# Optimization experiments

Measured on AMD Instinct MI355X. Metric: run time of the kernel, lower is better.

## Reference

```python
import jax, jax.numpy as jnp
import numpy as np

B, T, EMBED_DIM, HEAD_SIZE = 512, 256, 384, 64


def setup_inputs() -> dict:
    key = jax.random.key(0)
    k1, k2, k3, k4 = jax.random.split(key, 4)
    x = jax.random.normal(k1, (B, T, EMBED_DIM), dtype=jnp.float32)
    # torch nn.Linear(embed_dim, head_size, bias=False): y = x @ W.T with W [out,in].
    # We store W as [in, out] so the projection is x @ W.
    Wq = jax.random.normal(k2, (EMBED_DIM, HEAD_SIZE), dtype=jnp.float32) * 0.02
    Wk = jax.random.normal(k3, (EMBED_DIM, HEAD_SIZE), dtype=jnp.float32) * 0.02
    Wv = jax.random.normal(k4, (EMBED_DIM, HEAD_SIZE), dtype=jnp.float32) * 0.02
    return {"x": x, "Wq": Wq, "Wk": Wk, "Wv": Wv}


def reference(x, Wq, Wk, Wv):
    # x: [B, T, E]
    Tlen = x.shape[1]
    E = x.shape[2]
    q = x @ Wq  # [B, T, H]
    k = x @ Wk  # [B, T, H]
    v = x @ Wv  # [B, T, H]
    wei = jnp.einsum("bqh,bkh->bqk", q, k)  # [B, T, T] raw scores (no pre-softmax scale!)
    causal = jnp.tril(jnp.ones((Tlen, Tlen), dtype=bool))
    wei = jnp.where(causal, wei, jnp.float32(-jnp.inf))
    wei = jax.nn.softmax(wei, axis=-1)
    # NOTE: original module divides by sqrt(embed_dim) AFTER softmax (faithful quirk).
    wei = wei / jnp.sqrt(jnp.asarray(E, wei.dtype))
    # dropout is identity in eval/deterministic mode
    out = jnp.einsum("bqk,bkh->bqh", wei, v)  # [B, T, H]
    return out
```

## Files before the change

kernel.cpp:

```cpp
#include <hip/hip_runtime.h>


typedef _Float16 half8 __attribute__((ext_vector_type(8)));
typedef float f32x4 __attribute__((ext_vector_type(4)));

#define MFMA16(a, b, c) __builtin_amdgcn_mfma_f32_16x16x32_f16(a, b, c, 0, 0, 0)

#define QOFF 0
#define QSTR 72
#define KOFF 18432
#define VOFF 36864
#define VSTR 264
#define POFF 53760
#define PSTR 24
#define LDS_F16 59904
#define LDS_BYTES (LDS_F16 * 2)

__global__ void pack_w_kernel(const float* __restrict__ Wq, const float* __restrict__ Wk,
                              const float* __restrict__ Wv, _Float16* __restrict__ wp) {
    int tid = blockIdx.x * 256 + threadIdx.x;
    if (tid >= 12 * 12 * 64 * 8) return;
    int i    = tid & 7;
    int l    = (tid >> 3) & 63;
    int ctks = tid >> 9;
    int ct   = ctks % 12;
    int ks   = ctks / 12;
    int k    = ks * 32 + 8 * (l >> 4) + i;
    int c    = l & 15;
    const float* src;
    int h;
    if (ct < 4)      { src = Wq; h = ct * 16 + c; }
    else if (ct < 8) { src = Wk; h = (ct - 4) * 16 + c; }
    else             { src = Wv; h = (ct - 8) * 16 + c; }
    wp[tid] = (_Float16)src[k * 64 + h];
}

__global__ __launch_bounds__(512) void fused_kernel(
        const float* __restrict__ x, const _Float16* __restrict__ wp,
        float* __restrict__ out) {
    extern __shared__ _Float16 lds[];
    const int b = blockIdx.x;
    const int w = threadIdx.x >> 6, l = threadIdx.x & 63;
    const int c = l & 15, g = l >> 4;

    {
        const float* base0 = x + (b * 256 + w * 32 + c) * 384;
        const float* base1 = base0 + 16 * 384;
        f32x4 acc[2][12] = {};
        float4 buf[2][4];
        buf[0][0] = *(const float4*)(base0 + 8 * g);
        buf[0][1] = *(const float4*)(base0 + 8 * g + 4);
        buf[0][2] = *(const float4*)(base1 + 8 * g);
        buf[0][3] = *(const float4*)(base1 + 8 * g + 4);
#pragma unroll
        for (int s = 0; s < 12; ++s) {
            const int cb = s & 1, nb = cb ^ 1;
            if (s < 11) {
                int o = (s + 1) * 32 + 8 * g;
                buf[nb][0] = *(const float4*)(base0 + o);
                buf[nb][1] = *(const float4*)(base0 + o + 4);
                buf[nb][2] = *(const float4*)(base1 + o);
                buf[nb][3] = *(const float4*)(base1 + o + 4);
            }
            half8 a0, a1;
#pragma unroll
            for (int e = 0; e < 4; ++e) {
                a0[e]     = (_Float16)buf[cb][0][e];
                a0[e + 4] = (_Float16)buf[cb][1][e];
                a1[e]     = (_Float16)buf[cb][2][e];
                a1[e + 4] = (_Float16)buf[cb][3][e];
            }
#pragma unroll
            for (int ct = 0; ct < 12; ++ct) {
                half8 bf = *(const half8*)(wp + ((s * 12 + ct) * 64 + l) * 8);
                acc[0][ct] = MFMA16(a0, bf, acc[0][ct]);
                acc[1][ct] = MFMA16(a1, bf, acc[1][ct]);
            }
        }
#pragma unroll
        for (int rt = 0; rt < 2; ++rt) {
            int r0 = w * 32 + rt * 16;
#pragma unroll
            for (int ct = 0; ct < 12; ++ct) {
                if (ct < 4) {
                    int h = ct * 16 + c;
#pragma unroll
                    for (int r = 0; r < 4; ++r)
                        lds[QOFF + (r0 + 4 * g + r) * QSTR + h] = (_Float16)acc[rt][ct][r];
                } else if (ct < 8) {
                    int h = (ct - 4) * 16 + c;
#pragma unroll
                    for (int r = 0; r < 4; ++r)
                        lds[KOFF + (r0 + 4 * g + r) * QSTR + h] = (_Float16)acc[rt][ct][r];
                } else {
                    int h  = (ct - 8) * 16 + c;
                    int t0 = r0 + 4 * g;
                    union { ushort4 u; _Float16 hh[4]; } pk;
#pragma unroll
                    for (int r = 0; r < 4; ++r) pk.hh[r] = (_Float16)acc[rt][ct][r];
                    *(ushort4*)&lds[VOFF + h * VSTR + t0] = pk.u;
                }
            }
        }
    }
    __syncthreads();

    const float qk_scale = 0.05103103630798288f;
    float* ob = out + b * 16384;
    _Float16* pw = &lds[POFF + w * 768];

#pragma unroll
    for (int j = 0; j < 2; ++j) {
        const int qt = j ? (15 - w) : w;
        const int r0 = qt * 16;
        half8 aq0 = *(const half8*)&lds[QOFF + (r0 + c) * QSTR + 8 * g];
        half8 aq1 = *(const half8*)&lds[QOFF + (r0 + c) * QSTR + 32 + 8 * g];

        f32x4 oac[4] = {};
        float lsum[4] = {0.f, 0.f, 0.f, 0.f};
        const int nkk = (qt >> 1) + 1;

        for (int kk = 0; kk < nkk; ++kk) {
            const int c0 = kk * 32;
            f32x4 S[2];
#pragma unroll
            for (int t = 0; t < 2; ++t) {
                const _Float16* kp = &lds[KOFF + (c0 + 16 * t + c) * QSTR + 8 * g];
                half8 bk0 = *(const half8*)kp;
                half8 bk1 = *(const half8*)(kp + 32);
                f32x4 z = {};
                z = MFMA16(aq0, bk0, z);
                z = MFMA16(aq1, bk1, z);
                S[t] = z;
            }
            float p[2][4];
            if (kk == nkk - 1) {
#pragma unroll
                for (int t = 0; t < 2; ++t)
#pragma unroll
                    for (int r = 0; r < 4; ++r) {
                        float sv = (c0 + 16 * t + c > r0 + 4 * g + r) ? -1e30f
                                                                      : S[t][r] - 6.0f;
                        p[t][r] = __expf(sv);
                        lsum[r] += p[t][r];
                    }
            } else {
#pragma unroll
                for (int t = 0; t < 2; ++t)
#pragma unroll
                    for (int r = 0; r < 4; ++r) {
                        p[t][r] = __expf(S[t][r] - 6.0f);
                        lsum[r] += p[t][r];
                    }
            }
#pragma unroll
            for (int t = 0; t < 2; ++t)
#pragma unroll
                for (int r = 0; r < 4; ++r)
                    pw[t * 384 + (4 * g + r) * PSTR + c] = (_Float16)p[t][r];
            asm volatile("s_waitcnt lgkmcnt(0)" ::: "memory");
            half8 pa = *(const half8*)&pw[(g >> 1) * 384 + c * PSTR + 8 * (g & 1)];
#pragma unroll
            for (int ht = 0; ht < 4; ++ht) {
                half8 bv = *(const half8*)&lds[VOFF + (16 * ht + c) * VSTR + c0 + 8 * g];
                oac[ht] = MFMA16(pa, bv, oac[ht]);
            }
        }
#pragma unroll
        for (int r = 0; r < 4; ++r) {
            float ls = lsum[r];
            ls += __shfl_xor(ls, 1);
            ls += __shfl_xor(ls, 2);
            ls += __shfl_xor(ls, 4);
            ls += __shfl_xor(ls, 8);
            float inv = qk_scale / ls;
#pragma unroll
            for (int ht = 0; ht < 4; ++ht)
                ob[(r0 + 4 * g + r) * 64 + 16 * ht + c] = oac[ht][r] * inv;
        }
    }
}

extern "C" void kernel_launch(void* const* d_in, const int* in_sizes, int n_in,
                              void* d_out, int out_size, void* d_ws, size_t ws_size,
                              hipStream_t stream) {
    const float* x  = (const float*)d_in[0];
    const float* Wq = (const float*)d_in[1];
    const float* Wk = (const float*)d_in[2];
    const float* Wv = (const float*)d_in[3];
    float* out = (float*)d_out;
    _Float16* wp = (_Float16*)d_ws;

    (void)hipFuncSetAttribute((const void*)fused_kernel,
                              hipFuncAttributeMaxDynamicSharedMemorySize, LDS_BYTES);

    pack_w_kernel<<<288, 256, 0, stream>>>(Wq, Wk, Wv, wp);
    fused_kernel<<<512, 512, LDS_BYTES, stream>>>(x, wp, out);
}
```

Measured before the change: 333.3 us.

## Stage weights in LDS, swizzle Q/K/V layouts, transpose S to keep P in registers

Projection weights are now staged into LDS in two halves instead of being read from global memory per MFMA. x loads move to a three-deep buffer. Q/K/V go into XOR-swizzled, unpadded LDS layouts, which lowers bank conflicts and LDS footprint, and launch bounds ask for two blocks per CU. The attention part computes transposed scores (K·Q) so P can be repacked with cross-lane shuffles instead of a round trip through LDS. It also skips the fully masked half-tile on the diagonal and writes the output with vectorized stores. In exchange it adds extra barriers during the projection, shuffle overhead, and register pressure from the occupancy hint.

```diff
diff --git a/kernel.cpp b/kernel.cpp
--- a/kernel.cpp
+++ b/kernel.cpp
@@ -2,19 +2,32 @@
 
 
 typedef _Float16 half8 __attribute__((ext_vector_type(8)));
+typedef __fp16 fp16x2 __attribute__((ext_vector_type(2)));
 typedef float f32x4 __attribute__((ext_vector_type(4)));
 
 #define MFMA16(a, b, c) __builtin_amdgcn_mfma_f32_16x16x32_f16(a, b, c, 0, 0, 0)
 
 #define QOFF 0
-#define QSTR 72
-#define KOFF 18432
-#define VOFF 36864
-#define VSTR 264
-#define POFF 53760
-#define PSTR 24
-#define LDS_F16 59904
+#define KOFF 16384
+#define VOFF 32768
+#define LDS_F16 49152
 #define LDS_BYTES (LDS_F16 * 2)
+
+__device__ __forceinline__ int qk_idx(int row, int h) {
+    return row * 64 + (h & 7) + ((((h >> 3) ^ row) & 7) << 3);
+}
+__device__ __forceinline__ int vt_idx(int h, int key) {
+    return h * 256 + (key & 7) + ((((key >> 3) ^ (h & 7)) & 31) << 3);
+}
+
+__device__ __forceinline__ unsigned long long pkquad(float a, float b, float c, float d) {
+    fp16x2 lo = __builtin_amdgcn_cvt_pkrtz(a, b);
+    fp16x2 hi = __builtin_amdgcn_cvt_pkrtz(c, d);
+    unsigned ulo, uhi;
+    __builtin_memcpy(&ulo, &lo, 4);
+    __builtin_memcpy(&uhi, &hi, 4);
+    return ((unsigned long long)uhi << 32) | ulo;
+}
 
 __global__ void pack_w_kernel(const float* __restrict__ Wq, const float* __restrict__ Wk,
                               const float* __restrict__ Wv, _Float16* __restrict__ wp) {
@@ -24,8 +37,8 @@
     int l    = (tid >> 3) & 63;
     int ctks = tid >> 9;
     int ct   = ctks % 12;
-    int ks   = ctks / 12;
-    int k    = ks * 32 + 8 * (l >> 4) + i;
+    int s    = ctks / 12;
+    int k    = s * 32 + 8 * (l >> 4) + i;
     int c    = l & 15;
     const float* src;
     int h;
@@ -35,71 +48,84 @@
     wp[tid] = (_Float16)src[k * 64 + h];
 }
 
-__global__ __launch_bounds__(512) void fused_kernel(
+__global__ __launch_bounds__(512, 2) void fused_kernel(
         const float* __restrict__ x, const _Float16* __restrict__ wp,
         float* __restrict__ out) {
     extern __shared__ _Float16 lds[];
     const int b = blockIdx.x;
-    const int w = threadIdx.x >> 6, l = threadIdx.x & 63;
+    const int tid = threadIdx.x;
+    const int w = tid >> 6, l = tid & 63;
     const int c = l & 15, g = l >> 4;
 
-    {
-        const float* base0 = x + (b * 256 + w * 32 + c) * 384;
-        const float* base1 = base0 + 16 * 384;
-        f32x4 acc[2][12] = {};
-        float4 buf[2][4];
-        buf[0][0] = *(const float4*)(base0 + 8 * g);
-        buf[0][1] = *(const float4*)(base0 + 8 * g + 4);
-        buf[0][2] = *(const float4*)(base1 + 8 * g);
-        buf[0][3] = *(const float4*)(base1 + 8 * g + 4);
-#pragma unroll
-        for (int s = 0; s < 12; ++s) {
-            const int cb = s & 1, nb = cb ^ 1;
-            if (s < 11) {
-                int o = (s + 1) * 32 + 8 * g;
-                buf[nb][0] = *(const float4*)(base0 + o);
-                buf[nb][1] = *(const float4*)(base0 + o + 4);
-                buf[nb][2] = *(const float4*)(base1 + o);
-                buf[nb][3] = *(const float4*)(base1 + o + 4);
-            }
-            half8 a0, a1;
-#pragma unroll
-            for (int e = 0; e < 4; ++e) {
-                a0[e]     = (_Float16)buf[cb][0][e];
-                a0[e + 4] = (_Float16)buf[cb][1][e];
-                a1[e]     = (_Float16)buf[cb][2][e];
-                a1[e + 4] = (_Float16)buf[cb][3][e];
-            }
-#pragma unroll
-            for (int ct = 0; ct < 12; ++ct) {
-                half8 bf = *(const half8*)(wp + ((s * 12 + ct) * 64 + l) * 8);
-                acc[0][ct] = MFMA16(a0, bf, acc[0][ct]);
-                acc[1][ct] = MFMA16(a1, bf, acc[1][ct]);
-            }
-        }
-#pragma unroll
-        for (int rt = 0; rt < 2; ++rt) {
-            int r0 = w * 32 + rt * 16;
-#pragma unroll
-            for (int ct = 0; ct < 12; ++ct) {
-                if (ct < 4) {
-                    int h = ct * 16 + c;
-#pragma unroll
-                    for (int r = 0; r < 4; ++r)
-                        lds[QOFF + (r0 + 4 * g + r) * QSTR + h] = (_Float16)acc[rt][ct][r];
-                } else if (ct < 8) {
-                    int h = (ct - 4) * 16 + c;
-#pragma unroll
-                    for (int r = 0; r < 4; ++r)
-                        lds[KOFF + (r0 + 4 * g + r) * QSTR + h] = (_Float16)acc[rt][ct][r];
-                } else {
-                    int h  = (ct - 8) * 16 + c;
-                    int t0 = r0 + 4 * g;
-                    union { ushort4 u; _Float16 hh[4]; } pk;
-#pragma unroll
-                    for (int r = 0; r < 4; ++r) pk.hh[r] = (_Float16)acc[rt][ct][r];
-                    *(ushort4*)&lds[VOFF + h * VSTR + t0] = pk.u;
+    const float* base0 = x + (b * 256 + w * 32 + c) * 384;
+    const float* base1 = base0 + 16 * 384;
+    f32x4 acc[2][12] = {};
+
+#pragma unroll
+    for (int i = 0; i < 9; ++i) {
+        int ch = i * 512 + tid;
+        *(uint4*)&lds[ch * 8] = *(const uint4*)(wp + ch * 8);
+    }
+    __syncthreads();
+
+    f32x4 xb[3][4];
+#define XLOAD(bi, s) do { const float* p0_ = base0 + (s) * 32 + 8 * g; \
+        const float* p1_ = base1 + (s) * 32 + 8 * g; \
+        xb[bi][0] = *(const f32x4*)p0_; xb[bi][1] = *(const f32x4*)(p0_ + 4); \
+        xb[bi][2] = *(const f32x4*)p1_; xb[bi][3] = *(const f32x4*)(p1_ + 4); } while (0)
+
+    XLOAD(0, 0);
+    XLOAD(1, 1);
+#pragma unroll
+    for (int s = 0; s < 12; ++s) {
+        if (s == 6) {
+            __syncthreads();
+#pragma unroll
+            for (int i = 0; i < 9; ++i) {
+                int ch = i * 512 + tid;
+                *(uint4*)&lds[ch * 8] = *(const uint4*)(wp + 36864 + ch * 8);
+            }
+            __syncthreads();
+        }
+        const int cb = s % 3;
+        if (s < 10) XLOAD((s + 2) % 3, s + 2);
+        half8 a0, a1;
+#pragma unroll
+        for (int e = 0; e < 4; ++e) {
+            a0[e]     = (_Float16)xb[cb][0][e];
+            a0[e + 4] = (_Float16)xb[cb][1][e];
+            a1[e]     = (_Float16)xb[cb][2][e];
+            a1[e + 4] = (_Float16)xb[cb][3][e];
+        }
+#pragma unroll
+        for (int ct = 0; ct < 12; ++ct) {
+            half8 bf = *(const half8*)&lds[((s % 6) * 12 + ct) * 512 + l * 8];
+            acc[0][ct] = MFMA16(a0, bf, acc[0][ct]);
+            acc[1][ct] = MFMA16(a1, bf, acc[1][ct]);
+        }
+    }
+    __syncthreads();
+
+#pragma unroll
+    for (int rt = 0; rt < 2; ++rt) {
+        int r0 = w * 32 + rt * 16;
+#pragma unroll
+        for (int ct = 0; ct < 12; ++ct) {
+            if (ct < 8) {
+                int off = (ct < 4) ? QOFF : KOFF;
+                int h = (ct & 3) * 16 + c;
+#pragma unroll
+                for (int r = 0; r < 4; ++r) {
+                    int row = r0 + 4 * g + r;
+                    lds[off + qk_idx(row, h)] = (_Float16)acc[rt][ct][r];
                 }
+            } else {
+                int h  = (ct - 8) * 16 + c;
+                int t0 = r0 + 4 * g;
+                union { ushort4 u; _Float16 hh[4]; } pk;
+#pragma unroll
+                for (int r = 0; r < 4; ++r) pk.hh[r] = (_Float16)acc[rt][ct][r];
+                *(ushort4*)&lds[VOFF + vt_idx(h, t0)] = pk.u;
             }
         }
     }
@@ -107,76 +133,81 @@
 
     const float qk_scale = 0.05103103630798288f;
     float* ob = out + b * 16384;
-    _Float16* pw = &lds[POFF + w * 768];
 
 #pragma unroll
     for (int j = 0; j < 2; ++j) {
         const int qt = j ? (15 - w) : w;
         const int r0 = qt * 16;
-        half8 aq0 = *(const half8*)&lds[QOFF + (r0 + c) * QSTR + 8 * g];
-        half8 aq1 = *(const half8*)&lds[QOFF + (r0 + c) * QSTR + 32 + 8 * g];
-
-        f32x4 oac[4] = {};
-        float lsum[4] = {0.f, 0.f, 0.f, 0.f};
+        const int qrow = r0 + c;
+        half8 aq0 = *(const half8*)&lds[QOFF + qrow * 64 + (((g ^ qrow) & 7) << 3)];
+        half8 aq1 = *(const half8*)&lds[QOFF + qrow * 64 + ((((g + 4) ^ qrow) & 7) << 3)];
+
+        f32x4 oacT[4] = {};
+        float lsum = 0.f;
         const int nkk = (qt >> 1) + 1;
 
         for (int kk = 0; kk < nkk; ++kk) {
             const int c0 = kk * 32;
-            f32x4 S[2];
-#pragma unroll
-            for (int t = 0; t < 2; ++t) {
-                const _Float16* kp = &lds[KOFF + (c0 + 16 * t + c) * QSTR + 8 * g];
-                half8 bk0 = *(const half8*)kp;
-                half8 bk1 = *(const half8*)(kp + 32);
-                f32x4 z = {};
-                z = MFMA16(aq0, bk0, z);
-                z = MFMA16(aq1, bk1, z);
-                S[t] = z;
-            }
-            float p[2][4];
-            if (kk == nkk - 1) {
-#pragma unroll
-                for (int t = 0; t < 2; ++t)
-#pragma unroll
-                    for (int r = 0; r < 4; ++r) {
-                        float sv = (c0 + 16 * t + c > r0 + 4 * g + r) ? -1e30f
-                                                                      : S[t][r] - 6.0f;
-                        p[t][r] = __expf(sv);
-                        lsum[r] += p[t][r];
-                    }
-            } else {
-#pragma unroll
-                for (int t = 0; t < 2; ++t)
-#pragma unroll
-                    for (int r = 0; r < 4; ++r) {
-                        p[t][r] = __expf(S[t][r] - 6.0f);
-                        lsum[r] += p[t][r];
-                    }
-            }
-#pragma unroll
-            for (int t = 0; t < 2; ++t)
-#pragma unroll
-                for (int r = 0; r < 4; ++r)
-                    pw[t * 384 + (4 * g + r) * PSTR + c] = (_Float16)p[t][r];
-            asm volatile("s_waitcnt lgkmcnt(0)" ::: "memory");
-            half8 pa = *(const half8*)&pw[(g >> 1) * 384 + c * PSTR + 8 * (g & 1)];
+            const bool diag  = (kk == nkk - 1);
+            const bool skip1 = diag && !(qt & 1);
+            const bool m0    = diag && !(qt & 1);
+            const bool m1    = diag && (qt & 1);
+
+            f32x4 S0 = {}, S1 = {};
+            {
+                int krow = c0 + c;
+                half8 ak0 = *(const half8*)&lds[KOFF + krow * 64 + (((g ^ krow) & 7) << 3)];
+                half8 ak1 = *(const half8*)&lds[KOFF + krow * 64 + ((((g + 4) ^ krow) & 7) << 3)];
+                S0 = MFMA16(ak0, aq0, S0);
+                S0 = MFMA16(ak1, aq1, S0);
+            }
+            if (!skip1) {
+                int krow = c0 + 16 + c;
+                half8 ak0 = *(const half8*)&lds[KOFF + krow * 64 + (((g ^ krow) & 7) << 3)];
+                half8 ak1 = *(const half8*)&lds[KOFF + krow * 64 + ((((g + 4) ^ krow) & 7) << 3)];
+                S1 = MFMA16(ak0, aq0, S1);
+                S1 = MFMA16(ak1, aq1, S1);
+            }
+
+            float p0[4], p1[4];
+#pragma unroll
+            for (int r = 0; r < 4; ++r) {
+                float e0 = __expf(S0[r] - 6.0f);
+                p0[r] = (m0 && (4 * g + r > c)) ? 0.f : e0;
+                float e1 = __expf(S1[r] - 6.0f);
+                p1[r] = (skip1 || (m1 && (4 * g + r > c))) ? 0.f : e1;
+                lsum += p0[r] + p1[r];
+            }
+
+            unsigned long long A  = pkquad(p0[0], p0[1], p0[2], p0[3]);
+            unsigned long long Bq = pkquad(p1[0], p1[1], p1[2], p1[3]);
+            const bool ghi  = (g & 2) != 0;
+            const bool godd = (g & 1) != 0;
+            unsigned long long R1 = __shfl_xor(ghi ? A : Bq, 32, 64);
+            unsigned long long s2 = godd ? (ghi ? R1 : A) : (ghi ? Bq : R1);
+            unsigned long long R2 = __shfl_xor(s2, 16, 64);
+            unsigned long long d01 = godd ? R2 : (ghi ? R1 : A);
+            unsigned long long d23 = godd ? (ghi ? Bq : R1) : R2;
+            unsigned long long pbu[2] = {d01, d23};
+            half8 pb;
+            __builtin_memcpy(&pb, pbu, 16);
+
 #pragma unroll
             for (int ht = 0; ht < 4; ++ht) {
-                half8 bv = *(const half8*)&lds[VOFF + (16 * ht + c) * VSTR + c0 + 8 * g];
-                oac[ht] = MFMA16(pa, bv, oac[ht]);
-            }
-        }
-#pragma unroll
-        for (int r = 0; r < 4; ++r) {
-            float ls = lsum[r];
-            ls += __shfl_xor(ls, 1);
-            ls += __shfl_xor(ls, 2);
-            ls += __shfl_xor(ls, 4);
-            ls += __shfl_xor(ls, 8);
-            float inv = qk_scale / ls;
-#pragma unroll
-            for (int ht = 0; ht < 4; ++ht)
-                ob[(r0 + 4 * g + r) * 64 + 16 * ht + c] = oac[ht][r] * inv;
+                int hrow = 16 * ht + c;
+                half8 av = *(const half8*)&lds[VOFF + hrow * 256 +
+                              ((((c0 >> 3) + g) ^ (c & 7)) << 3)];
+                oacT[ht] = MFMA16(av, pb, oacT[ht]);
+            }
+        }
+
+        lsum += __shfl_xor(lsum, 16, 64);
+        lsum += __shfl_xor(lsum, 32, 64);
+        float inv = qk_scale / lsum;
+#pragma unroll
+        for (int ht = 0; ht < 4; ++ht) {
+            f32x4 sv = oacT[ht] * inv;
+            *(f32x4*)&ob[qrow * 64 + 16 * ht + 4 * g] = sv;
         }
     }
 }
```

Result: faster. 310.0 us (-7.0%).
